# Performance work log

Hardware: AMD Instinct MI355X
Metric: run time of the kernel (lower is better)

## Reference

```python
import jax, jax.numpy as jnp
import numpy as np

TEMPERATURE = 8.0  # sqrt(d_k), d_k = 64


def setup_inputs() -> dict:
    key = jax.random.key(0)
    kq, kk, kv, km = jax.random.split(key, 4)
    B, Lq, Lk, D = 64, 1024, 1024, 64
    q = jax.random.normal(kq, (B, Lq, D), dtype=jnp.float32)
    k = jax.random.normal(kk, (B, Lk, D), dtype=jnp.float32)
    v = jax.random.normal(kv, (B, Lk, D), dtype=jnp.float32)
    mask = jax.random.randint(km, (B, Lq, Lk), 0, 2).astype(jnp.bool_)
    return {"q": q, "k": k, "v": v, "mask": mask}


def reference(q, k, v, mask):
    # attn = q @ k^T / temperature, masked softmax over last dim, then @ v
    attn = jnp.einsum("bqd,bkd->bqk", q, k) / TEMPERATURE
    attn = jnp.where(mask, -jnp.inf, attn)
    attn = jax.nn.softmax(attn, axis=2)
    output = jnp.einsum("bqk,bkd->bqd", attn, v)
    return (output, attn)
```

## Files before the change

### kernel.cpp

```cpp
#include <hip/hip_runtime.h>
#include <hip/hip_bf16.h>


typedef __attribute__((ext_vector_type(8))) short bf16x8;
typedef __attribute__((ext_vector_type(4))) short bf16x4;
typedef __attribute__((ext_vector_type(4))) float f32x4;
typedef __attribute__((ext_vector_type(4))) int   i32x4;

#define GLOBAL_AS __attribute__((address_space(1)))
#define LDS_AS    __attribute__((address_space(3)))

static __device__ __forceinline__ short f2bf(float f) {
    return (short)__builtin_bit_cast(unsigned short, __float2bfloat16(f));
}
static __device__ __forceinline__ bf16x8 pack8(float4 a, float4 b) {
    union { bf16x8 v; __hip_bfloat162 h[4]; } u;
    u.h[0] = __float22bfloat162_rn(make_float2(a.x, a.y));
    u.h[1] = __float22bfloat162_rn(make_float2(a.z, a.w));
    u.h[2] = __float22bfloat162_rn(make_float2(b.x, b.y));
    u.h[3] = __float22bfloat162_rn(make_float2(b.z, b.w));
    return u.v;
}
static __device__ __forceinline__ bf16x8 pack8v(f32x4 a, f32x4 b) {
    union { bf16x8 v; __hip_bfloat162 h[4]; } u;
    u.h[0] = __float22bfloat162_rn(make_float2(a[0], a[1]));
    u.h[1] = __float22bfloat162_rn(make_float2(a[2], a[3]));
    u.h[2] = __float22bfloat162_rn(make_float2(b[0], b[1]));
    u.h[3] = __float22bfloat162_rn(make_float2(b[2], b[3]));
    return u.v;
}
static __device__ __forceinline__ bf16x4 pack4(float a, float b, float c, float d) {
    union { bf16x4 v; __hip_bfloat162 h[2]; } u;
    u.h[0] = __float22bfloat162_rn(make_float2(a, b));
    u.h[1] = __float22bfloat162_rn(make_float2(c, d));
    return u.v;
}
static __device__ __forceinline__ f32x4 vscale(f32x4 a, float s) {
    a[0] *= s; a[1] *= s; a[2] *= s; a[3] *= s; return a;
}

static __device__ __forceinline__ void dma16(void* lds, const void* g) {
    __builtin_amdgcn_global_load_lds((const GLOBAL_AS unsigned*)g,
                                     (LDS_AS unsigned*)lds, 16, 0, 0);
}
static __device__ __forceinline__ void stage8k(short* lds, const short* g, int w, int L) {
    dma16((void*)(lds + (w * 2 + 0) * 512), (const void*)(g + (w * 2 + 0) * 512 + L * 8));
    dma16((void*)(lds + (w * 2 + 1) * 512), (const void*)(g + (w * 2 + 1) * 512 + L * 8));
}

__global__ __launch_bounds__(256) void pre_kv(const float* __restrict__ k,
                                              const float* __restrict__ v,
                                              short* __restrict__ kb,
                                              short* __restrict__ vt) {
    __shared__ short t[64][72];
    const int tid = threadIdx.x;
    if (blockIdx.x < 2048) {
        long ci = (long)blockIdx.x * 256 + tid;
        long row = ci >> 3;
        int  c   = (int)(ci & 7);
        const f32x4* s = (const f32x4*)(k + row * 64 + c * 8);
        f32x4 a  = __builtin_nontemporal_load(s);
        f32x4 b2 = __builtin_nontemporal_load(s + 1);
        int r = (int)(row & 63);
        short* dst = kb + (row >> 6) * 4096 + (long)r * 64 + ((c ^ (r & 7)) << 3);
        *(bf16x8*)dst = pack8v(a, b2);
    } else {
        const int bkt = blockIdx.x - 2048;
        const int row = tid >> 2;
        const int cg  = (tid & 3) * 16;
        const float* src = v + ((long)bkt * 64 + row) * 64 + cg;
        f32x4 f0 = __builtin_nontemporal_load((const f32x4*)src);
        f32x4 f1 = __builtin_nontemporal_load((const f32x4*)src + 1);
        f32x4 f2 = __builtin_nontemporal_load((const f32x4*)src + 2);
        f32x4 f3 = __builtin_nontemporal_load((const f32x4*)src + 3);
        float vv[16] = {f0[0], f0[1], f0[2], f0[3], f1[0], f1[1], f1[2], f1[3],
                        f2[0], f2[1], f2[2], f2[3], f3[0], f3[1], f3[2], f3[3]};
        #pragma unroll
        for (int dd = 0; dd < 16; ++dd) t[cg + dd][row] = f2bf(vv[dd]);
        __syncthreads();
        const int d = tid >> 2, c0 = (tid & 3) * 2;
        short* dstrow = vt + (long)bkt * 4096 + d * 64;
        *(int4*)&dstrow[((c0 ^ (d & 7)) << 3)]       = *(int4*)&t[d][c0 * 8];
        *(int4*)&dstrow[(((c0 + 1) ^ (d & 7)) << 3)] = *(int4*)&t[d][c0 * 8 + 8];
    }
}

__global__ __launch_bounds__(256, 4) void attn_main(
    const float* __restrict__ q, const int* __restrict__ mask,
    unsigned long long* __restrict__ bits,
    const short* __restrict__ kb, const short* __restrict__ vt,
    float* __restrict__ out, float* __restrict__ attn)
{
    __shared__ short kbuf[2][4096];
    __shared__ short vbuf[2][4096];
    __shared__ short ptile[4][1024];

    const int tid  = threadIdx.x;
    const int w    = tid >> 6;
    const int L    = tid & 63;
    const int n    = L & 15;
    const int g    = L >> 4;
    const int lin  = blockIdx.x;
    const int b    = (lin & 7) * 8 + ((lin >> 3) >> 4);
    const int qt   = (lin >> 3) & 15;
    const long bq  = (long)b * 1024 + qt * 64;

    const short* ktg = kb + (long)b * 65536;
    const short* vtg = vt + (long)b * 65536;

    const long grow = bq + 16 * w + n;

    const float* qrow = q + grow * 64 + g * 8;
    f32x4 qa0 = ((const f32x4*)qrow)[0];
    f32x4 qa1 = ((const f32x4*)qrow)[1];
    f32x4 qb0 = ((const f32x4*)(qrow + 32))[0];
    f32x4 qb1 = ((const f32x4*)(qrow + 32))[1];
    const float sc = 0.125f * 1.4426950408889634f;
    qa0 = vscale(qa0, sc); qa1 = vscale(qa1, sc);
    qb0 = vscale(qb0, sc); qb1 = vscale(qb1, sc);
    bf16x8 qf0 = pack8v(qa0, qa1);
    bf16x8 qf1 = pack8v(qb0, qb1);

    const int* mbase = mask + grow * 1024 + g * 4;
    const int sw = (n & 7);

    float lp = 0.f;
    stage8k(kbuf[0], ktg, w, L);
    __syncthreads();

    for (int kt = 0; kt < 16; ++kt) {
        if (kt < 15) {
            stage8k(kbuf[(kt + 1) & 1], ktg + (kt + 1) * 4096, w, L);
        } else {
            stage8k(kbuf[0], ktg, w, L);
            stage8k(vbuf[0], vtg, w, L);
        }
        const int* mp = mbase + kt * 64;
        i32x4 mm0 = __builtin_nontemporal_load((const i32x4*)(mp));
        i32x4 mm1 = __builtin_nontemporal_load((const i32x4*)(mp + 16));
        i32x4 mm2 = __builtin_nontemporal_load((const i32x4*)(mp + 32));
        i32x4 mm3 = __builtin_nontemporal_load((const i32x4*)(mp + 48));

        const short* kl = kbuf[kt & 1];
        f32x4 acc[4];
        #pragma unroll
        for (int t = 0; t < 4; ++t) { acc[t][0]=0.f; acc[t][1]=0.f; acc[t][2]=0.f; acc[t][3]=0.f; }
        #pragma unroll
        for (int t = 0; t < 4; ++t) {
            bf16x8 kf0 = *(const bf16x8*)&kl[(t * 16 + n) * 64 + ((g ^ sw) << 3)];
            bf16x8 kf1 = *(const bf16x8*)&kl[(t * 16 + n) * 64 + (((4 + g) ^ sw) << 3)];
            acc[t] = __builtin_amdgcn_mfma_f32_16x16x32_bf16(kf0, qf0, acc[t], 0, 0, 0);
            acc[t] = __builtin_amdgcn_mfma_f32_16x16x32_bf16(kf1, qf1, acc[t], 0, 0, 0);
        }
        unsigned nb[4];
        nb[0] = (mm0[0]!=0?1u:0u)|(mm0[1]!=0?2u:0u)|(mm0[2]!=0?4u:0u)|(mm0[3]!=0?8u:0u);
        nb[1] = (mm1[0]!=0?1u:0u)|(mm1[1]!=0?2u:0u)|(mm1[2]!=0?4u:0u)|(mm1[3]!=0?8u:0u);
        nb[2] = (mm2[0]!=0?1u:0u)|(mm2[1]!=0?2u:0u)|(mm2[2]!=0?4u:0u)|(mm2[3]!=0?8u:0u);
        nb[3] = (mm3[0]!=0?1u:0u)|(mm3[1]!=0?2u:0u)|(mm3[2]!=0?4u:0u)|(mm3[3]!=0?8u:0u);
        #pragma unroll
        for (int t = 0; t < 4; ++t)
            #pragma unroll
            for (int i = 0; i < 4; ++i)
                lp += ((nb[t] >> i) & 1u) ? 0.f : __builtin_exp2f(acc[t][i]);
        unsigned long long wword =
              ((unsigned long long)nb[0] << (g * 4))
            | ((unsigned long long)nb[1] << (16 + g * 4))
            | ((unsigned long long)nb[2] << (32 + g * 4))
            | ((unsigned long long)nb[3] << (48 + g * 4));
        wword |= __shfl_xor(wword, 16);
        wword |= __shfl_xor(wword, 32);
        if (g == 0) bits[grow * 16 + kt] = wword;
        __syncthreads();
    }
    float l = lp + __shfl_xor(lp, 16);
    l += __shfl_xor(l, 32);
    const float linv = 1.0f / l;

    f32x4 oacc[4];
    #pragma unroll
    for (int u = 0; u < 4; ++u) { oacc[u][0]=0.f; oacc[u][1]=0.f; oacc[u][2]=0.f; oacc[u][3]=0.f; }

    const unsigned long long* mrow_ptr = bits + grow * 16;
    float* attn_row = attn + grow * 1024;
    short* pw = ptile[w];

    for (int kt = 0; kt < 16; ++kt) {
        if (kt < 15) {
            stage8k(kbuf[(kt + 1) & 1], ktg + (kt + 1) * 4096, w, L);
            stage8k(vbuf[(kt + 1) & 1], vtg + (kt + 1) * 4096, w, L);
        }
        unsigned long long mrow = mrow_ptr[kt];
        const short* kl = kbuf[kt & 1];
        const short* vl = vbuf[kt & 1];
        f32x4 acc[4];
        #pragma unroll
        for (int t = 0; t < 4; ++t) { acc[t][0]=0.f; acc[t][1]=0.f; acc[t][2]=0.f; acc[t][3]=0.f; }
        #pragma unroll
        for (int t = 0; t < 4; ++t) {
            bf16x8 kf0 = *(const bf16x8*)&kl[(t * 16 + n) * 64 + ((g ^ sw) << 3)];
            bf16x8 kf1 = *(const bf16x8*)&kl[(t * 16 + n) * 64 + (((4 + g) ^ sw) << 3)];
            acc[t] = __builtin_amdgcn_mfma_f32_16x16x32_bf16(kf0, qf0, acc[t], 0, 0, 0);
            acc[t] = __builtin_amdgcn_mfma_f32_16x16x32_bf16(kf1, qf1, acc[t], 0, 0, 0);
        }
        unsigned long long ms = mrow >> (g * 4);
        #pragma unroll
        for (int t = 0; t < 4; ++t) {
            unsigned b0 = (unsigned)(ms >> (t * 16 + 0)) & 1u;
            unsigned b1 = (unsigned)(ms >> (t * 16 + 1)) & 1u;
            unsigned b2 = (unsigned)(ms >> (t * 16 + 2)) & 1u;
            unsigned b3 = (unsigned)(ms >> (t * 16 + 3)) & 1u;
            float p0 = b0 ? 0.f : __builtin_exp2f(acc[t][0]) * linv;
            float p1 = b1 ? 0.f : __builtin_exp2f(acc[t][1]) * linv;
            float p2 = b2 ? 0.f : __builtin_exp2f(acc[t][2]) * linv;
            float p3 = b3 ? 0.f : __builtin_exp2f(acc[t][3]) * linv;
            f32x4 pv; pv[0] = p0; pv[1] = p1; pv[2] = p2; pv[3] = p3;
            __builtin_nontemporal_store(pv, (f32x4*)(attn_row + kt * 64 + t * 16 + g * 4));
            *(bf16x4*)&pw[n * 64 + ((((t * 2) + (g >> 1)) ^ sw) << 3) + (g & 1) * 4] =
                pack4(p0, p1, p2, p3);
        }
        bf16x8 pf0 = *(const bf16x8*)&pw[n * 64 + ((g ^ sw) << 3)];
        bf16x8 pf1 = *(const bf16x8*)&pw[n * 64 + (((4 + g) ^ sw) << 3)];
        #pragma unroll
        for (int u = 0; u < 4; ++u) {
            bf16x8 vf0 = *(const bf16x8*)&vl[(u * 16 + n) * 64 + ((g ^ sw) << 3)];
            bf16x8 vf1 = *(const bf16x8*)&vl[(u * 16 + n) * 64 + (((4 + g) ^ sw) << 3)];
            oacc[u] = __builtin_amdgcn_mfma_f32_16x16x32_bf16(pf0, vf0, oacc[u], 0, 0, 0);
            oacc[u] = __builtin_amdgcn_mfma_f32_16x16x32_bf16(pf1, vf1, oacc[u], 0, 0, 0);
        }
        __syncthreads();
    }

    #pragma unroll
    for (int u = 0; u < 4; ++u)
        #pragma unroll
        for (int i = 0; i < 4; ++i)
            __builtin_nontemporal_store(oacc[u][i],
                &out[(bq + 16 * w + g * 4 + i) * 64 + u * 16 + n]);
}

#define KSTRIDE 72
#define PSTRIDE 68
__global__ __launch_bounds__(256) void attn_fallback(
    const float* __restrict__ q, const float* __restrict__ k,
    const float* __restrict__ v, const int* __restrict__ mask,
    float* __restrict__ out, float* __restrict__ attn)
{
    __shared__ unsigned maskbits[64][32];
    __shared__ short kbuf[64 * KSTRIDE];
    __shared__ short vtbuf[64 * KSTRIDE];
    __shared__ float ptilef[4 * 16 * PSTRIDE];

    const int tid  = threadIdx.x;
    const int w    = tid >> 6;
    const int L    = tid & 63;
    const int n    = L & 15;
    const int quad = L >> 4;
    const int b    = blockIdx.y;
    const long bq  = (long)b * 1024 + blockIdx.x * 64;

    const float* qrow = q + (bq + 16 * w + n) * 64 + quad * 8;
    float4 qa0 = ((const float4*)qrow)[0];
    float4 qa1 = ((const float4*)(qrow + 4))[0];
    float4 qb0 = ((const float4*)(qrow + 32))[0];
    float4 qb1 = ((const float4*)(qrow + 36))[0];
    const float sc = 0.125f;
    qa0.x *= sc; qa0.y *= sc; qa0.z *= sc; qa0.w *= sc;
    qa1.x *= sc; qa1.y *= sc; qa1.z *= sc; qa1.w *= sc;
    qb0.x *= sc; qb0.y *= sc; qb0.z *= sc; qb0.w *= sc;
    qb1.x *= sc; qb1.y *= sc; qb1.z *= sc; qb1.w *= sc;
    bf16x8 qf0 = pack8(qa0, qa1);
    bf16x8 qf1 = pack8(qb0, qb1);

    #pragma unroll
    for (int ii = 0; ii < 8; ++ii) {
        int wi  = ii * 256 + tid;
        int row = wi >> 5;
        int wc  = wi & 31;
        const int4* mp = (const int4*)(mask + (bq + row) * 1024 + wc * 32);
        unsigned word = 0;
        #pragma unroll
        for (int j = 0; j < 8; ++j) {
            int4 m4 = mp[j];
            word |= (m4.x != 0 ? 1u : 0u) << (4 * j + 0);
            word |= (m4.y != 0 ? 1u : 0u) << (4 * j + 1);
            word |= (m4.z != 0 ? 1u : 0u) << (4 * j + 2);
            word |= (m4.w != 0 ? 1u : 0u) << (4 * j + 3);
        }
        maskbits[row][wc] = word;
    }

    float m_i[4] = {-1e30f, -1e30f, -1e30f, -1e30f};
    float l_i[4] = {0.f, 0.f, 0.f, 0.f};

    for (int kt = 0; kt < 16; ++kt) {
        __syncthreads();
        {
            const float* kr = k + ((long)b * 1024 + kt * 64 + L) * 64 + w * 16;
            float4 k0 = ((const float4*)kr)[0];
            float4 k1 = ((const float4*)kr)[1];
            float4 k2 = ((const float4*)kr)[2];
            float4 k3 = ((const float4*)kr)[3];
            bf16x8* dst = (bf16x8*)&kbuf[L * KSTRIDE + w * 16];
            dst[0] = pack8(k0, k1);
            dst[1] = pack8(k2, k3);
        }
        __syncthreads();
        f32x4 acc[4];
        #pragma unroll
        for (int t = 0; t < 4; ++t) { acc[t][0]=0.f; acc[t][1]=0.f; acc[t][2]=0.f; acc[t][3]=0.f; }
        #pragma unroll
        for (int t = 0; t < 4; ++t) {
            bf16x8 b0 = *(const bf16x8*)&kbuf[(t * 16 + n) * KSTRIDE + quad * 8];
            bf16x8 b1 = *(const bf16x8*)&kbuf[(t * 16 + n) * KSTRIDE + 32 + quad * 8];
            acc[t] = __builtin_amdgcn_mfma_f32_16x16x32_bf16(qf0, b0, acc[t], 0, 0, 0);
            acc[t] = __builtin_amdgcn_mfma_f32_16x16x32_bf16(qf1, b1, acc[t], 0, 0, 0);
        }
        #pragma unroll
        for (int i = 0; i < 4; ++i) {
            int mrow = 16 * w + quad * 4 + i;
            unsigned w0 = maskbits[mrow][kt * 2];
            unsigned w1 = maskbits[mrow][kt * 2 + 1];
            float s0 = ((w0 >> n)        & 1u) ? -1e30f : acc[0][i];
            float s1 = ((w0 >> (16 + n)) & 1u) ? -1e30f : acc[1][i];
            float s2 = ((w1 >> n)        & 1u) ? -1e30f : acc[2][i];
            float s3 = ((w1 >> (16 + n)) & 1u) ? -1e30f : acc[3][i];
            float mt = fmaxf(fmaxf(s0, s1), fmaxf(s2, s3));
            mt = fmaxf(mt, __shfl_xor(mt, 1));
            mt = fmaxf(mt, __shfl_xor(mt, 2));
            mt = fmaxf(mt, __shfl_xor(mt, 4));
            mt = fmaxf(mt, __shfl_xor(mt, 8));
            float mnew = fmaxf(m_i[i], mt);
            float ps = __expf(s0 - mnew) + __expf(s1 - mnew)
                     + __expf(s2 - mnew) + __expf(s3 - mnew);
            ps += __shfl_xor(ps, 1);
            ps += __shfl_xor(ps, 2);
            ps += __shfl_xor(ps, 4);
            ps += __shfl_xor(ps, 8);
            l_i[i] = l_i[i] * __expf(m_i[i] - mnew) + ps;
            m_i[i] = mnew;
        }
    }
    float linv[4];
    #pragma unroll
    for (int i = 0; i < 4; ++i) linv[i] = 1.0f / l_i[i];

    f32x4 oacc[4];
    #pragma unroll
    for (int t = 0; t < 4; ++t) { oacc[t][0]=0.f; oacc[t][1]=0.f; oacc[t][2]=0.f; oacc[t][3]=0.f; }
    float* attn_row = attn + (bq + 16 * w + n) * 1024;

    for (int kt = 0; kt < 16; ++kt) {
        __syncthreads();
        {
            const float* kr = k + ((long)b * 1024 + kt * 64 + L) * 64 + w * 16;
            float4 k0 = ((const float4*)kr)[0];
            float4 k1 = ((const float4*)kr)[1];
            float4 k2 = ((const float4*)kr)[2];
            float4 k3 = ((const float4*)kr)[3];
            bf16x8* dst = (bf16x8*)&kbuf[L * KSTRIDE + w * 16];
            dst[0] = pack8(k0, k1);
            dst[1] = pack8(k2, k3);
            const float* vr = v + ((long)b * 1024 + kt * 64 + L) * 64 + w * 16;
            float4 v0 = ((const float4*)vr)[0];
            float4 v1 = ((const float4*)vr)[1];
            float4 v2 = ((const float4*)vr)[2];
            float4 v3 = ((const float4*)vr)[3];
            float vv[16] = {v0.x, v0.y, v0.z, v0.w, v1.x, v1.y, v1.z, v1.w,
                            v2.x, v2.y, v2.z, v2.w, v3.x, v3.y, v3.z, v3.w};
            #pragma unroll
            for (int dd = 0; dd < 16; ++dd)
                vtbuf[(w * 16 + dd) * KSTRIDE + L] = f2bf(vv[dd]);
        }
        __syncthreads();
        f32x4 acc[4];
        #pragma unroll
        for (int t = 0; t < 4; ++t) { acc[t][0]=0.f; acc[t][1]=0.f; acc[t][2]=0.f; acc[t][3]=0.f; }
        #pragma unroll
        for (int t = 0; t < 4; ++t) {
            bf16x8 b0 = *(const bf16x8*)&kbuf[(t * 16 + n) * KSTRIDE + quad * 8];
            bf16x8 b1 = *(const bf16x8*)&kbuf[(t * 16 + n) * KSTRIDE + 32 + quad * 8];
            acc[t] = __builtin_amdgcn_mfma_f32_16x16x32_bf16(qf0, b0, acc[t], 0, 0, 0);
            acc[t] = __builtin_amdgcn_mfma_f32_16x16x32_bf16(qf1, b1, acc[t], 0, 0, 0);
        }
        #pragma unroll
        for (int i = 0; i < 4; ++i) {
            int mrow = 16 * w + quad * 4 + i;
            unsigned w0 = maskbits[mrow][kt * 2];
            unsigned w1 = maskbits[mrow][kt * 2 + 1];
            float s0 = ((w0 >> n)        & 1u) ? -1e30f : acc[0][i];
            float s1 = ((w0 >> (16 + n)) & 1u) ? -1e30f : acc[1][i];
            float s2 = ((w1 >> n)        & 1u) ? -1e30f : acc[2][i];
            float s3 = ((w1 >> (16 + n)) & 1u) ? -1e30f : acc[3][i];
            float* pr = &ptilef[(w * 16 + quad * 4 + i) * PSTRIDE];
            pr[n]      = __expf(s0 - m_i[i]) * linv[i];
            pr[16 + n] = __expf(s1 - m_i[i]) * linv[i];
            pr[32 + n] = __expf(s2 - m_i[i]) * linv[i];
            pr[48 + n] = __expf(s3 - m_i[i]) * linv[i];
        }
        bf16x8 pf[2];
        #pragma unroll
        for (int c = 0; c < 2; ++c) {
            const float* pp = &ptilef[(w * 16 + n) * PSTRIDE + c * 32 + quad * 8];
            float4 p0 = ((const float4*)pp)[0];
            float4 p1 = ((const float4*)pp)[1];
            float* ap = attn_row + kt * 64 + c * 32 + quad * 8;
            ((float4*)ap)[0] = p0;
            ((float4*)ap)[1] = p1;
            pf[c] = pack8(p0, p1);
        }
        #pragma unroll
        for (int t = 0; t < 4; ++t) {
            bf16x8 vb0 = *(const bf16x8*)&vtbuf[(t * 16 + n) * KSTRIDE + quad * 8];
            bf16x8 vb1 = *(const bf16x8*)&vtbuf[(t * 16 + n) * KSTRIDE + 32 + quad * 8];
            oacc[t] = __builtin_amdgcn_mfma_f32_16x16x32_bf16(pf[0], vb0, oacc[t], 0, 0, 0);
            oacc[t] = __builtin_amdgcn_mfma_f32_16x16x32_bf16(pf[1], vb1, oacc[t], 0, 0, 0);
        }
    }
    #pragma unroll
    for (int t = 0; t < 4; ++t)
        #pragma unroll
        for (int i = 0; i < 4; ++i)
            out[(bq + 16 * w + quad * 4 + i) * 64 + t * 16 + n] = oacc[t][i];
}

extern "C" void kernel_launch(void* const* d_in, const int* in_sizes, int n_in,
                              void* d_out, int out_size, void* d_ws, size_t ws_size,
                              hipStream_t stream) {
    const float* q    = (const float*)d_in[0];
    const float* k    = (const float*)d_in[1];
    const float* v    = (const float*)d_in[2];
    const int*   mask = (const int*)d_in[3];
    float* out  = (float*)d_out;
    float* attn = out + (long)64 * 1024 * 64;

    const size_t need = (size_t)24 << 20;
    if (ws_size >= need) {
        unsigned char* ws = (unsigned char*)d_ws;
        unsigned long long* bits = (unsigned long long*)ws;
        short* kbw = (short*)(ws + ((size_t)8 << 20));
        short* vtw = (short*)(ws + ((size_t)16 << 20));
        pre_kv<<<3072, 256, 0, stream>>>(k, v, kbw, vtw);
        attn_main<<<dim3(1024, 1, 1), dim3(256, 1, 1), 0, stream>>>(
            q, mask, bits, kbw, vtw, out, attn);
    } else {
        attn_fallback<<<dim3(16, 64, 1), dim3(256, 1, 1), 0, stream>>>(
            q, k, v, mask, out, attn);
    }
}
```

Measured before the change: 538.5 us.

## Deepen first-pass K staging to four buffers and prefetch mask two tiles ahead

The K and V LDS buffers are merged into one four-slot buffer. The first (row-sum) pass now stages K two tiles ahead and keeps mask loads in flight two iterations ahead in registers. That lets it sync only every other iteration. The second pass prefetches the next mask bitword one iteration early. The aim is to hide global mask and K latency and to cut barriers, at the cost of more registers, which may reduce occupancy.

```diff
diff --git a/kernel.cpp b/kernel.cpp
--- a/kernel.cpp
+++ b/kernel.cpp
@@ -91,8 +91,7 @@
     const short* __restrict__ kb, const short* __restrict__ vt,
     float* __restrict__ out, float* __restrict__ attn)
 {
-    __shared__ short kbuf[2][4096];
-    __shared__ short vbuf[2][4096];
+    __shared__ short sbuf[4][4096];
     __shared__ short ptile[4][1024];
 
     const int tid  = threadIdx.x;
@@ -125,23 +124,32 @@
     const int sw = (n & 7);
 
     float lp = 0.f;
-    stage8k(kbuf[0], ktg, w, L);
+    stage8k(sbuf[0], ktg, w, L);
+    stage8k(sbuf[1], ktg + 4096, w, L);
+    i32x4 ma0 = __builtin_nontemporal_load((const i32x4*)(mbase));
+    i32x4 ma1 = __builtin_nontemporal_load((const i32x4*)(mbase + 16));
+    i32x4 ma2 = __builtin_nontemporal_load((const i32x4*)(mbase + 32));
+    i32x4 ma3 = __builtin_nontemporal_load((const i32x4*)(mbase + 48));
+    i32x4 mb0 = __builtin_nontemporal_load((const i32x4*)(mbase + 64));
+    i32x4 mb1 = __builtin_nontemporal_load((const i32x4*)(mbase + 80));
+    i32x4 mb2 = __builtin_nontemporal_load((const i32x4*)(mbase + 96));
+    i32x4 mb3 = __builtin_nontemporal_load((const i32x4*)(mbase + 112));
     __syncthreads();
 
+    #pragma unroll 2
     for (int kt = 0; kt < 16; ++kt) {
-        if (kt < 15) {
-            stage8k(kbuf[(kt + 1) & 1], ktg + (kt + 1) * 4096, w, L);
-        } else {
-            stage8k(kbuf[0], ktg, w, L);
-            stage8k(vbuf[0], vtg, w, L);
-        }
-        const int* mp = mbase + kt * 64;
-        i32x4 mm0 = __builtin_nontemporal_load((const i32x4*)(mp));
-        i32x4 mm1 = __builtin_nontemporal_load((const i32x4*)(mp + 16));
-        i32x4 mm2 = __builtin_nontemporal_load((const i32x4*)(mp + 32));
-        i32x4 mm3 = __builtin_nontemporal_load((const i32x4*)(mp + 48));
-
-        const short* kl = kbuf[kt & 1];
+        if (kt < 14)       stage8k(sbuf[(kt + 2) & 3], ktg + (kt + 2) * 4096, w, L);
+        else if (kt == 14) stage8k(sbuf[0], ktg, w, L);
+        else               stage8k(sbuf[2], vtg, w, L);
+        i32x4 mc0 = {}, mc1 = {}, mc2 = {}, mc3 = {};
+        if (kt < 14) {
+            const int* mp = mbase + (kt + 2) * 64;
+            mc0 = __builtin_nontemporal_load((const i32x4*)(mp));
+            mc1 = __builtin_nontemporal_load((const i32x4*)(mp + 16));
+            mc2 = __builtin_nontemporal_load((const i32x4*)(mp + 32));
+            mc3 = __builtin_nontemporal_load((const i32x4*)(mp + 48));
+        }
+        const short* kl = sbuf[kt & 3];
         f32x4 acc[4];
         #pragma unroll
         for (int t = 0; t < 4; ++t) { acc[t][0]=0.f; acc[t][1]=0.f; acc[t][2]=0.f; acc[t][3]=0.f; }
@@ -153,10 +161,10 @@
             acc[t] = __builtin_amdgcn_mfma_f32_16x16x32_bf16(kf1, qf1, acc[t], 0, 0, 0);
         }
         unsigned nb[4];
-        nb[0] = (mm0[0]!=0?1u:0u)|(mm0[1]!=0?2u:0u)|(mm0[2]!=0?4u:0u)|(mm0[3]!=0?8u:0u);
-        nb[1] = (mm1[0]!=0?1u:0u)|(mm1[1]!=0?2u:0u)|(mm1[2]!=0?4u:0u)|(mm1[3]!=0?8u:0u);
-        nb[2] = (mm2[0]!=0?1u:0u)|(mm2[1]!=0?2u:0u)|(mm2[2]!=0?4u:0u)|(mm2[3]!=0?8u:0u);
-        nb[3] = (mm3[0]!=0?1u:0u)|(mm3[1]!=0?2u:0u)|(mm3[2]!=0?4u:0u)|(mm3[3]!=0?8u:0u);
+        nb[0] = (ma0[0]!=0?1u:0u)|(ma0[1]!=0?2u:0u)|(ma0[2]!=0?4u:0u)|(ma0[3]!=0?8u:0u);
+        nb[1] = (ma1[0]!=0?1u:0u)|(ma1[1]!=0?2u:0u)|(ma1[2]!=0?4u:0u)|(ma1[3]!=0?8u:0u);
+        nb[2] = (ma2[0]!=0?1u:0u)|(ma2[1]!=0?2u:0u)|(ma2[2]!=0?4u:0u)|(ma2[3]!=0?8u:0u);
+        nb[3] = (ma3[0]!=0?1u:0u)|(ma3[1]!=0?2u:0u)|(ma3[2]!=0?4u:0u)|(ma3[3]!=0?8u:0u);
         #pragma unroll
         for (int t = 0; t < 4; ++t)
             #pragma unroll
@@ -170,7 +178,9 @@
         wword |= __shfl_xor(wword, 16);
         wword |= __shfl_xor(wword, 32);
         if (g == 0) bits[grow * 16 + kt] = wword;
-        __syncthreads();
+        ma0 = mb0; ma1 = mb1; ma2 = mb2; ma3 = mb3;
+        mb0 = mc0; mb1 = mc1; mb2 = mc2; mb3 = mc3;
+        if ((kt & 1) || kt >= 14) __syncthreads();
     }
     float l = lp + __shfl_xor(lp, 16);
     l += __shfl_xor(l, 32);
@@ -183,15 +193,17 @@
     const unsigned long long* mrow_ptr = bits + grow * 16;
     float* attn_row = attn + grow * 1024;
     short* pw = ptile[w];
+    unsigned long long mcur = mrow_ptr[0];
 
     for (int kt = 0; kt < 16; ++kt) {
         if (kt < 15) {
-            stage8k(kbuf[(kt + 1) & 1], ktg + (kt + 1) * 4096, w, L);
-            stage8k(vbuf[(kt + 1) & 1], vtg + (kt + 1) * 4096, w, L);
-        }
-        unsigned long long mrow = mrow_ptr[kt];
-        const short* kl = kbuf[kt & 1];
-        const short* vl = vbuf[kt & 1];
+            stage8k(sbuf[(kt + 1) & 1],       ktg + (kt + 1) * 4096, w, L);
+            stage8k(sbuf[2 + ((kt + 1) & 1)], vtg + (kt + 1) * 4096, w, L);
+        }
+        unsigned long long mnext = 0;
+        if (kt < 15) mnext = mrow_ptr[kt + 1];
+        const short* kl = sbuf[kt & 1];
+        const short* vl = sbuf[2 + (kt & 1)];
         f32x4 acc[4];
         #pragma unroll
         for (int t = 0; t < 4; ++t) { acc[t][0]=0.f; acc[t][1]=0.f; acc[t][2]=0.f; acc[t][3]=0.f; }
@@ -202,7 +214,7 @@
             acc[t] = __builtin_amdgcn_mfma_f32_16x16x32_bf16(kf0, qf0, acc[t], 0, 0, 0);
             acc[t] = __builtin_amdgcn_mfma_f32_16x16x32_bf16(kf1, qf1, acc[t], 0, 0, 0);
         }
-        unsigned long long ms = mrow >> (g * 4);
+        unsigned long long ms = mcur >> (g * 4);
         #pragma unroll
         for (int t = 0; t < 4; ++t) {
             unsigned b0 = (unsigned)(ms >> (t * 16 + 0)) & 1u;
@@ -227,6 +239,7 @@
             oacc[u] = __builtin_amdgcn_mfma_f32_16x16x32_bf16(pf0, vf0, oacc[u], 0, 0, 0);
             oacc[u] = __builtin_amdgcn_mfma_f32_16x16x32_bf16(pf1, vf1, oacc[u], 0, 0, 0);
         }
+        mcur = mnext;
         __syncthreads();
     }
 
```

New measurement: 556.2 us. 1.03x slower.

## Replace global_load_lds DMA with register-staged K/V prefetch and lgkm barrier

Applied to the files above, without the earlier changes.

Drops the direct global-to-LDS DMA loads. K/V tiles for the next iteration are now loaded into registers at the top of each loop and written to LDS just before a custom barrier that waits only on lgkmcnt. It also prefetches the next mask bit word one iteration early. The aim is to avoid the vmcnt drain that __syncthreads forces on the many outstanding nontemporal mask loads and attn stores. The cost is extra VGPRs and explicit LDS store instructions.

```diff
diff --git a/kernel.cpp b/kernel.cpp
--- a/kernel.cpp
+++ b/kernel.cpp
@@ -39,13 +39,10 @@
     a[0] *= s; a[1] *= s; a[2] *= s; a[3] *= s; return a;
 }
 
-static __device__ __forceinline__ void dma16(void* lds, const void* g) {
-    __builtin_amdgcn_global_load_lds((const GLOBAL_AS unsigned*)g,
-                                     (LDS_AS unsigned*)lds, 16, 0, 0);
-}
-static __device__ __forceinline__ void stage8k(short* lds, const short* g, int w, int L) {
-    dma16((void*)(lds + (w * 2 + 0) * 512), (const void*)(g + (w * 2 + 0) * 512 + L * 8));
-    dma16((void*)(lds + (w * 2 + 1) * 512), (const void*)(g + (w * 2 + 1) * 512 + L * 8));
+static __device__ __forceinline__ void barrier_lgkm() {
+    asm volatile("s_waitcnt lgkmcnt(0)" ::: "memory");
+    __builtin_amdgcn_sched_barrier(0);
+    __builtin_amdgcn_s_barrier();
 }
 
 __global__ __launch_bounds__(256) void pre_kv(const float* __restrict__ k,
@@ -109,6 +106,7 @@
     const short* vtg = vt + (long)b * 65536;
 
     const long grow = bq + 16 * w + n;
+    const int so = (w * 2) * 512 + L * 8;
 
     const float* qrow = q + grow * 64 + g * 8;
     f32x4 qa0 = ((const f32x4*)qrow)[0];
@@ -124,16 +122,24 @@
     const int* mbase = mask + grow * 1024 + g * 4;
     const int sw = (n & 7);
 
+    {
+        bf16x8 k0 = *(const bf16x8*)(ktg + so);
+        bf16x8 k1 = *(const bf16x8*)(ktg + so + 512);
+        *(bf16x8*)(kbuf[0] + so)       = k0;
+        *(bf16x8*)(kbuf[0] + so + 512) = k1;
+    }
+    barrier_lgkm();
+
     float lp = 0.f;
-    stage8k(kbuf[0], ktg, w, L);
-    __syncthreads();
-
     for (int kt = 0; kt < 16; ++kt) {
-        if (kt < 15) {
-            stage8k(kbuf[(kt + 1) & 1], ktg + (kt + 1) * 4096, w, L);
-        } else {
-            stage8k(kbuf[0], ktg, w, L);
-            stage8k(vbuf[0], vtg, w, L);
+        const int nt = (kt < 15) ? kt + 1 : 0;
+        const short* ksrc = ktg + nt * 4096;
+        bf16x8 kr0 = *(const bf16x8*)(ksrc + so);
+        bf16x8 kr1 = *(const bf16x8*)(ksrc + so + 512);
+        bf16x8 vr0, vr1;
+        if (kt == 15) {
+            vr0 = *(const bf16x8*)(vtg + so);
+            vr1 = *(const bf16x8*)(vtg + so + 512);
         }
         const int* mp = mbase + kt * 64;
         i32x4 mm0 = __builtin_nontemporal_load((const i32x4*)(mp));
@@ -170,7 +176,14 @@
         wword |= __shfl_xor(wword, 16);
         wword |= __shfl_xor(wword, 32);
         if (g == 0) bits[grow * 16 + kt] = wword;
-        __syncthreads();
+        short* kd = kbuf[nt & 1];
+        *(bf16x8*)(kd + so)       = kr0;
+        *(bf16x8*)(kd + so + 512) = kr1;
+        if (kt == 15) {
+            *(bf16x8*)(vbuf[0] + so)       = vr0;
+            *(bf16x8*)(vbuf[0] + so + 512) = vr1;
+        }
+        barrier_lgkm();
     }
     float l = lp + __shfl_xor(lp, 16);
     l += __shfl_xor(l, 32);
@@ -183,13 +196,20 @@
     const unsigned long long* mrow_ptr = bits + grow * 16;
     float* attn_row = attn + grow * 1024;
     short* pw = ptile[w];
+    unsigned long long mcur = mrow_ptr[0];
 
     for (int kt = 0; kt < 16; ++kt) {
+        bf16x8 kr0, kr1, vr0, vr1;
+        unsigned long long mnext = 0;
         if (kt < 15) {
-            stage8k(kbuf[(kt + 1) & 1], ktg + (kt + 1) * 4096, w, L);
-            stage8k(vbuf[(kt + 1) & 1], vtg + (kt + 1) * 4096, w, L);
-        }
-        unsigned long long mrow = mrow_ptr[kt];
+            const short* ksrc = ktg + (kt + 1) * 4096;
+            const short* vsrc = vtg + (kt + 1) * 4096;
+            kr0 = *(const bf16x8*)(ksrc + so);
+            kr1 = *(const bf16x8*)(ksrc + so + 512);
+            vr0 = *(const bf16x8*)(vsrc + so);
+            vr1 = *(const bf16x8*)(vsrc + so + 512);
+            mnext = mrow_ptr[kt + 1];
+        }
         const short* kl = kbuf[kt & 1];
         const short* vl = vbuf[kt & 1];
         f32x4 acc[4];
@@ -202,7 +222,7 @@
             acc[t] = __builtin_amdgcn_mfma_f32_16x16x32_bf16(kf0, qf0, acc[t], 0, 0, 0);
             acc[t] = __builtin_amdgcn_mfma_f32_16x16x32_bf16(kf1, qf1, acc[t], 0, 0, 0);
         }
-        unsigned long long ms = mrow >> (g * 4);
+        unsigned long long ms = mcur >> (g * 4);
         #pragma unroll
         for (int t = 0; t < 4; ++t) {
             unsigned b0 = (unsigned)(ms >> (t * 16 + 0)) & 1u;
@@ -227,7 +247,16 @@
             oacc[u] = __builtin_amdgcn_mfma_f32_16x16x32_bf16(pf0, vf0, oacc[u], 0, 0, 0);
             oacc[u] = __builtin_amdgcn_mfma_f32_16x16x32_bf16(pf1, vf1, oacc[u], 0, 0, 0);
         }
-        __syncthreads();
+        if (kt < 15) {
+            short* kd = kbuf[(kt + 1) & 1];
+            short* vd = vbuf[(kt + 1) & 1];
+            *(bf16x8*)(kd + so)       = kr0;
+            *(bf16x8*)(kd + so + 512) = kr1;
+            *(bf16x8*)(vd + so)       = vr0;
+            *(bf16x8*)(vd + so + 512) = vr1;
+            barrier_lgkm();
+        }
+        mcur = mnext;
     }
 
     #pragma unroll
```

Result: slower. 570.3 us (+5.9%).
